# Kernel optimization log

Measured on AMD Instinct MI355X. Metric: run time of the kernel, lower is better.

Reference implementation:

```python
import jax, jax.numpy as jnp
import numpy as np

B, NINP, NCLS = 16384, 2048, 100


def setup_inputs() -> dict:
    key = jax.random.key(0)
    k1, k2, k3, k4, k5 = jax.random.split(key, 5)
    s = 1.0 / np.sqrt(NINP)
    return {
        "time_series": jax.random.normal(k1, (B, NINP), jnp.float32),
        "w_weight": jax.random.uniform(k2, (NINP, NINP), jnp.float32, -s, s),
        "w_bias": jax.random.uniform(k3, (NINP,), jnp.float32, -s, s),
        "fc_weight": jax.random.uniform(k4, (NCLS, NINP), jnp.float32, -s, s),
        "fc_bias": jax.random.uniform(k5, (NCLS,), jnp.float32, -s, s),
    }


def reference(time_series, w_weight, w_bias, fc_weight, fc_bias):
    # time_series: [B, N]
    n = time_series.shape[1]
    # gamma = cumsum(softmax(w(x), axis=1), axis=1): monotone warp in (0, 1]
    gamma = jnp.cumsum(jax.nn.softmax(time_series @ w_weight.T + w_bias, axis=1), axis=1)
    # Interp1d(linspace(0,1,N), x, gamma): per-row linear interpolation,
    # sampling each series at the warped time points gamma.
    xs = jnp.linspace(0.0, 1.0, n, dtype=time_series.dtype)  # shared knot grid
    warped = jax.vmap(lambda g, y: jnp.interp(g, xs, y))(gamma, time_series)  # [B, N]
    return warped @ fc_weight.T + fc_bias  # [B, nclasses]
```

## Files before the change

### kernel.cpp

```cpp
#include <hip/hip_runtime.h>
#include <hip/hip_bf16.h>

#define BROWS 16384
#define NDIM  2048
#define NCLS  100

typedef __attribute__((ext_vector_type(8))) __bf16 bf16x8;
typedef __attribute__((ext_vector_type(4))) float f32x4;
typedef __attribute__((ext_vector_type(4))) unsigned short u16x4;
typedef __attribute__((ext_vector_type(8))) unsigned short u16x8;

__device__ __forceinline__ unsigned short f2bf(float f) {
    union { float f; unsigned int u; } v; v.f = f;
    unsigned int u = v.u;
    unsigned int r = (u + 0x7fffu + ((u >> 16) & 1u)) >> 16;
    return (unsigned short)r;
}
__device__ __forceinline__ float bf2f(unsigned short h) {
    union { unsigned int u; float f; } v; v.u = ((unsigned int)h) << 16;
    return v.f;
}

#define GLOAD_LDS(g, l) \
    __builtin_amdgcn_global_load_lds((const __attribute__((address_space(1))) void*)(g), \
                                     (__attribute__((address_space(3))) void*)(l), 16, 0, 0)

__global__ __launch_bounds__(256) void split_kernel(const float4* __restrict__ src,
                                                    u16x4* __restrict__ hi,
                                                    u16x4* __restrict__ lo, int n4)
{
    int i = blockIdx.x * 256 + threadIdx.x;
    if (i >= n4) return;
    float4 v = src[i];
    u16x4 h, l;
    h.x = f2bf(v.x); l.x = f2bf(v.x - bf2f(h.x));
    h.y = f2bf(v.y); l.y = f2bf(v.y - bf2f(h.y));
    h.z = f2bf(v.z); l.z = f2bf(v.z - bf2f(h.z));
    h.w = f2bf(v.w); l.w = f2bf(v.w - bf2f(h.w));
    hi[i] = h; lo[i] = l;
}

__global__ __launch_bounds__(256) void cvt_bf16_kernel(const float4* __restrict__ src,
                                                       u16x4* __restrict__ dst, int n4)
{
    int i = blockIdx.x * 256 + threadIdx.x;
    if (i >= n4) return;
    float4 v = src[i];
    u16x4 h;
    h.x = f2bf(v.x); h.y = f2bf(v.y); h.z = f2bf(v.z); h.w = f2bf(v.w);
    dst[i] = h;
}

__global__ __launch_bounds__(256) void gemm1_mfma_fused_kernel(
        const unsigned short* __restrict__ xhi,
        const unsigned short* __restrict__ xlo,
        const unsigned short* __restrict__ whi,
        const unsigned short* __restrict__ wlo,
        const float* __restrict__ bias,
        float* __restrict__ C)
{
    __shared__ unsigned short sAh[128 * 32];
    __shared__ unsigned short sAl[128 * 32];
    __shared__ unsigned short sBh[128 * 32];
    __shared__ unsigned short sBl[128 * 32];

    const int tid  = threadIdx.x;
    const int lane = tid & 63;
    const int w    = tid >> 6;
    const int wm   = w & 1;
    const int wn   = w >> 1;
    const int m0   = blockIdx.y * 128;
    const int n0   = blockIdx.x * 128;

    const int c0 = w * 128 + lane;
    const int r0 = c0 >> 2;
    const int q0 = (c0 & 3) ^ ((r0 >> 1) & 3);
    const int c1 = c0 + 64;
    const int r1 = c1 >> 2;
    const int q1 = (c1 & 3) ^ ((r1 >> 1) & 3);

    const size_t a_goff0 = (size_t)(m0 + r0) * NDIM + q0 * 8;
    const size_t a_goff1 = (size_t)(m0 + r1) * NDIM + q1 * 8;
    const size_t b_goff0 = (size_t)(n0 + r0) * NDIM + q0 * 8;
    const size_t b_goff1 = (size_t)(n0 + r1) * NDIM + q1 * 8;

    unsigned short* ldsAh0 = &sAh[w * 1024];   unsigned short* ldsAh1 = &sAh[w * 1024 + 512];
    unsigned short* ldsAl0 = &sAl[w * 1024];   unsigned short* ldsAl1 = &sAl[w * 1024 + 512];
    unsigned short* ldsBh0 = &sBh[w * 1024];   unsigned short* ldsBh1 = &sBh[w * 1024 + 512];
    unsigned short* ldsBl0 = &sBl[w * 1024];   unsigned short* ldsBl1 = &sBl[w * 1024 + 512];

    const int lm = lane & 15;
    const int lk = lane >> 4;
    int offA[4], offB[4];
#pragma unroll
    for (int i = 0; i < 4; i++) {
        int ra = wm * 64 + i * 16 + lm;
        offA[i] = ra * 32 + ((lk ^ ((ra >> 1) & 3)) * 8);
        int rb = wn * 64 + i * 16 + lm;
        offB[i] = rb * 32 + ((lk ^ ((rb >> 1) & 3)) * 8);
    }

    f32x4 acc[4][4];
#pragma unroll
    for (int i = 0; i < 4; i++)
#pragma unroll
        for (int j = 0; j < 4; j++) acc[i][j] = (f32x4){0.f, 0.f, 0.f, 0.f};

    for (int kt = 0; kt < NDIM; kt += 32) {
        GLOAD_LDS(xhi + a_goff0 + kt, ldsAh0);
        GLOAD_LDS(xhi + a_goff1 + kt, ldsAh1);
        GLOAD_LDS(xlo + a_goff0 + kt, ldsAl0);
        GLOAD_LDS(xlo + a_goff1 + kt, ldsAl1);
        GLOAD_LDS(whi + b_goff0 + kt, ldsBh0);
        GLOAD_LDS(whi + b_goff1 + kt, ldsBh1);
        GLOAD_LDS(wlo + b_goff0 + kt, ldsBl0);
        GLOAD_LDS(wlo + b_goff1 + kt, ldsBl1);
        __syncthreads();

        bf16x8 ah[4], al[4], bh[4], bl[4];
#pragma unroll
        for (int i = 0; i < 4; i++) {
            ah[i] = *(const bf16x8*)&sAh[offA[i]];
            al[i] = *(const bf16x8*)&sAl[offA[i]];
            bh[i] = *(const bf16x8*)&sBh[offB[i]];
            bl[i] = *(const bf16x8*)&sBl[offB[i]];
        }
#pragma unroll
        for (int i = 0; i < 4; i++)
#pragma unroll
            for (int j = 0; j < 4; j++) {
                acc[i][j] = __builtin_amdgcn_mfma_f32_16x16x32_bf16(ah[i], bh[j], acc[i][j], 0, 0, 0);
                acc[i][j] = __builtin_amdgcn_mfma_f32_16x16x32_bf16(ah[i], bl[j], acc[i][j], 0, 0, 0);
                acc[i][j] = __builtin_amdgcn_mfma_f32_16x16x32_bf16(al[i], bh[j], acc[i][j], 0, 0, 0);
            }
        __syncthreads();
    }

    const int cn = lane & 15;
    const int rg = lane >> 4;
    float bb[4];
#pragma unroll
    for (int j = 0; j < 4; j++) bb[j] = bias[n0 + wn * 64 + j * 16 + cn];
#pragma unroll
    for (int i = 0; i < 4; i++) {
#pragma unroll
        for (int j = 0; j < 4; j++) {
            const int n = n0 + wn * 64 + j * 16 + cn;
#pragma unroll
            for (int reg = 0; reg < 4; reg++) {
                const int m = m0 + wm * 64 + i * 16 + rg * 4 + reg;
                C[(size_t)m * NDIM + n] = acc[i][j][reg] + bb[j];
            }
        }
    }
}

__global__ __launch_bounds__(256) void warp_bf16_kernel(const float* __restrict__ X,
                                                        const float* __restrict__ L,
                                                        unsigned short* __restrict__ Wout)
{
    const int N = NDIM;
    const int row = blockIdx.x;
    const int tid = threadIdx.x;
    const int lane = tid & 63;
    const int wave = tid >> 6;

    __shared__ float s_x[NDIM];
    __shared__ float s_red[4];
    __shared__ float s_wsum[4];

    const float* lrow = L + (size_t)row * N;
    const float* xrow = X + (size_t)row * N;

    float v[8];
    {
        float4 l0 = *(const float4*)(lrow + tid * 8);
        float4 l1 = *(const float4*)(lrow + tid * 8 + 4);
        v[0] = l0.x; v[1] = l0.y; v[2] = l0.z; v[3] = l0.w;
        v[4] = l1.x; v[5] = l1.y; v[6] = l1.z; v[7] = l1.w;
        float4 x0 = *(const float4*)(xrow + tid * 8);
        float4 x1 = *(const float4*)(xrow + tid * 8 + 4);
        *(float4*)&s_x[tid * 8]     = x0;
        *(float4*)&s_x[tid * 8 + 4] = x1;
    }

    float mx = v[0];
#pragma unroll
    for (int j = 1; j < 8; j++) mx = fmaxf(mx, v[j]);
#pragma unroll
    for (int off = 32; off > 0; off >>= 1) mx = fmaxf(mx, __shfl_down(mx, off));
    if (lane == 0) s_red[wave] = mx;
    __syncthreads();
    mx = fmaxf(fmaxf(s_red[0], s_red[1]), fmaxf(s_red[2], s_red[3]));

    float c = 0.0f;
#pragma unroll
    for (int j = 0; j < 8; j++) {
        float e = __expf(v[j] - mx);
        c += e;
        v[j] = c;
    }

    float sc = c;
#pragma unroll
    for (int off = 1; off < 64; off <<= 1) {
        float t = __shfl_up(sc, off);
        if (lane >= off) sc += t;
    }
    if (lane == 63) s_wsum[wave] = sc;
    __syncthreads();
    float base = 0.0f, total = 0.0f;
#pragma unroll
    for (int w = 0; w < 4; w++) {
        float t = s_wsum[w];
        if (w < wave) base += t;
        total += t;
    }
    const float inv = 1.0f / total;
    const float prefix = base + (sc - c);

    u16x8 o;
#pragma unroll
    for (int j = 0; j < 8; j++) {
        float g = (prefix + v[j]) * inv;
        float pos = g * (float)(N - 1);
        pos = fminf(fmaxf(pos, 0.0f), (float)(N - 1));
        int i = (int)pos;
        if (i > N - 2) i = N - 2;
        float f = pos - (float)i;
        o[j] = f2bf(fmaf(f, s_x[i + 1] - s_x[i], s_x[i]));
    }
    *(u16x8*)(Wout + (size_t)row * N + tid * 8) = o;
}

__global__ __launch_bounds__(256) void gemm2_mfma_kernel(
        const unsigned short* __restrict__ Wp,
        const unsigned short* __restrict__ F,
        const float* __restrict__ fb,
        float* __restrict__ out)
{
    __shared__ unsigned short sA[64 * 32];
    __shared__ unsigned short sB[128 * 32];

    const int tid  = threadIdx.x;
    const int lane = tid & 63;
    const int w    = tid >> 6;
    const int wm   = w & 1;
    const int wn   = w >> 1;
    const int m0   = blockIdx.x * 64;

    const int ca = w * 64 + lane;
    const int ra = ca >> 2;
    const int qa = (ca & 3) ^ ((ra >> 1) & 3);
    const size_t a_goff = (size_t)(m0 + ra) * NDIM + qa * 8;
    unsigned short* ldsA = &sA[w * 512];

    const int cb0 = w * 128 + lane;
    const int rb0 = cb0 >> 2;
    const int qb0 = (cb0 & 3) ^ ((rb0 >> 1) & 3);
    const int cb1 = cb0 + 64;
    const int rb1 = cb1 >> 2;
    const int qb1 = (cb1 & 3) ^ ((rb1 >> 1) & 3);
    const size_t b_goff0 = (size_t)(rb0 < NCLS ? rb0 : NCLS - 1) * NDIM + qb0 * 8;
    const size_t b_goff1 = (size_t)(rb1 < NCLS ? rb1 : NCLS - 1) * NDIM + qb1 * 8;
    unsigned short* ldsB0 = &sB[w * 1024];
    unsigned short* ldsB1 = &sB[w * 1024 + 512];

    const int lm = lane & 15;
    const int lk = lane >> 4;
    int offA[2], offB[4];
#pragma unroll
    for (int i = 0; i < 2; i++) {
        int r = wm * 32 + i * 16 + lm;
        offA[i] = r * 32 + ((lk ^ ((r >> 1) & 3)) * 8);
    }
#pragma unroll
    for (int j = 0; j < 4; j++) {
        int r = wn * 64 + j * 16 + lm;
        offB[j] = r * 32 + ((lk ^ ((r >> 1) & 3)) * 8);
    }

    f32x4 acc[2][4];
#pragma unroll
    for (int i = 0; i < 2; i++)
#pragma unroll
        for (int j = 0; j < 4; j++) acc[i][j] = (f32x4){0.f, 0.f, 0.f, 0.f};

    for (int kt = 0; kt < NDIM; kt += 32) {
        GLOAD_LDS(Wp + a_goff + kt, ldsA);
        GLOAD_LDS(F + b_goff0 + kt, ldsB0);
        GLOAD_LDS(F + b_goff1 + kt, ldsB1);
        __syncthreads();

        bf16x8 af[2], bf[4];
#pragma unroll
        for (int i = 0; i < 2; i++) af[i] = *(const bf16x8*)&sA[offA[i]];
#pragma unroll
        for (int j = 0; j < 4; j++) bf[j] = *(const bf16x8*)&sB[offB[j]];
#pragma unroll
        for (int i = 0; i < 2; i++)
#pragma unroll
            for (int j = 0; j < 4; j++)
                acc[i][j] = __builtin_amdgcn_mfma_f32_16x16x32_bf16(af[i], bf[j], acc[i][j], 0, 0, 0);
        __syncthreads();
    }

    const int cn = lane & 15;
    const int rg = lane >> 4;
#pragma unroll
    for (int i = 0; i < 2; i++) {
#pragma unroll
        for (int j = 0; j < 4; j++) {
            const int n = wn * 64 + j * 16 + cn;
            if (n < NCLS) {
                const float bbn = fb[n];
#pragma unroll
                for (int reg = 0; reg < 4; reg++) {
                    const int m = m0 + wm * 32 + i * 16 + rg * 4 + reg;
                    out[(size_t)m * NCLS + n] = acc[i][j][reg] + bbn;
                }
            }
        }
    }
}

__global__ __launch_bounds__(256) void gemm1_kernel(const float* __restrict__ X,
                                                    const float* __restrict__ W,
                                                    const float* __restrict__ bias,
                                                    float* __restrict__ C)
{
    const int K = NDIM;
    __shared__ float sA[16][128];
    __shared__ float sB[16][128];
    const int tid = threadIdx.x;
    const int tx = tid & 15;
    const int ty = tid >> 4;
    const int m0 = blockIdx.y * 128;
    const int n0 = blockIdx.x * 128;
    float acc[8][8];
#pragma unroll
    for (int i = 0; i < 8; i++)
#pragma unroll
        for (int j = 0; j < 8; j++) acc[i][j] = 0.0f;
    const int s_m = tid >> 1;
    const int s_c = (tid & 1) * 8;
    const float* Ag = X + (size_t)(m0 + s_m) * K + s_c;
    const float* Bg = W + (size_t)(n0 + s_m) * K + s_c;
    for (int kt = 0; kt < K; kt += 16) {
        float4 av0 = *(const float4*)(Ag + kt);
        float4 av1 = *(const float4*)(Ag + kt + 4);
        float4 bv0 = *(const float4*)(Bg + kt);
        float4 bv1 = *(const float4*)(Bg + kt + 4);
        __syncthreads();
        sA[s_c + 0][s_m] = av0.x; sA[s_c + 1][s_m] = av0.y;
        sA[s_c + 2][s_m] = av0.z; sA[s_c + 3][s_m] = av0.w;
        sA[s_c + 4][s_m] = av1.x; sA[s_c + 5][s_m] = av1.y;
        sA[s_c + 6][s_m] = av1.z; sA[s_c + 7][s_m] = av1.w;
        sB[s_c + 0][s_m] = bv0.x; sB[s_c + 1][s_m] = bv0.y;
        sB[s_c + 2][s_m] = bv0.z; sB[s_c + 3][s_m] = bv0.w;
        sB[s_c + 4][s_m] = bv1.x; sB[s_c + 5][s_m] = bv1.y;
        sB[s_c + 6][s_m] = bv1.z; sB[s_c + 7][s_m] = bv1.w;
        __syncthreads();
#pragma unroll
        for (int k = 0; k < 16; k++) {
            float4 a0 = *(const float4*)&sA[k][ty * 8];
            float4 a1 = *(const float4*)&sA[k][ty * 8 + 4];
            float4 b0 = *(const float4*)&sB[k][tx * 8];
            float4 b1 = *(const float4*)&sB[k][tx * 8 + 4];
            float a[8] = {a0.x, a0.y, a0.z, a0.w, a1.x, a1.y, a1.z, a1.w};
            float b[8] = {b0.x, b0.y, b0.z, b0.w, b1.x, b1.y, b1.z, b1.w};
#pragma unroll
            for (int i = 0; i < 8; i++)
#pragma unroll
                for (int j = 0; j < 8; j++)
                    acc[i][j] = fmaf(a[i], b[j], acc[i][j]);
        }
    }
    float bb[8];
#pragma unroll
    for (int j = 0; j < 8; j++) bb[j] = bias[n0 + tx * 8 + j];
#pragma unroll
    for (int i = 0; i < 8; i++) {
        const int m = m0 + ty * 8 + i;
        float* crow = C + (size_t)m * NDIM + n0 + tx * 8;
        *(float4*)(crow)     = make_float4(acc[i][0] + bb[0], acc[i][1] + bb[1],
                                           acc[i][2] + bb[2], acc[i][3] + bb[3]);
        *(float4*)(crow + 4) = make_float4(acc[i][4] + bb[4], acc[i][5] + bb[5],
                                           acc[i][6] + bb[6], acc[i][7] + bb[7]);
    }
}

__global__ __launch_bounds__(256) void warp_kernel_f32(const float* __restrict__ X,
                                                       float* __restrict__ L)
{
    const int N = NDIM;
    const int row = blockIdx.x;
    const int tid = threadIdx.x;
    const int lane = tid & 63;
    const int wave = tid >> 6;
    __shared__ float s_x[NDIM];
    __shared__ float s_red[4];
    __shared__ float s_wsum[4];
    float* lrow = L + (size_t)row * N;
    const float* xrow = X + (size_t)row * N;
    float v[8];
    {
        float4 l0 = *(const float4*)(lrow + tid * 8);
        float4 l1 = *(const float4*)(lrow + tid * 8 + 4);
        v[0] = l0.x; v[1] = l0.y; v[2] = l0.z; v[3] = l0.w;
        v[4] = l1.x; v[5] = l1.y; v[6] = l1.z; v[7] = l1.w;
        float4 x0 = *(const float4*)(xrow + tid * 8);
        float4 x1 = *(const float4*)(xrow + tid * 8 + 4);
        *(float4*)&s_x[tid * 8]     = x0;
        *(float4*)&s_x[tid * 8 + 4] = x1;
    }
    float mx = v[0];
#pragma unroll
    for (int j = 1; j < 8; j++) mx = fmaxf(mx, v[j]);
#pragma unroll
    for (int off = 32; off > 0; off >>= 1) mx = fmaxf(mx, __shfl_down(mx, off));
    if (lane == 0) s_red[wave] = mx;
    __syncthreads();
    mx = fmaxf(fmaxf(s_red[0], s_red[1]), fmaxf(s_red[2], s_red[3]));
    float c = 0.0f;
#pragma unroll
    for (int j = 0; j < 8; j++) {
        float e = __expf(v[j] - mx);
        c += e;
        v[j] = c;
    }
    float sc = c;
#pragma unroll
    for (int off = 1; off < 64; off <<= 1) {
        float t = __shfl_up(sc, off);
        if (lane >= off) sc += t;
    }
    if (lane == 63) s_wsum[wave] = sc;
    __syncthreads();
    float base = 0.0f, total = 0.0f;
#pragma unroll
    for (int w = 0; w < 4; w++) {
        float t = s_wsum[w];
        if (w < wave) base += t;
        total += t;
    }
    const float inv = 1.0f / total;
    const float prefix = base + (sc - c);
    float w8[8];
#pragma unroll
    for (int j = 0; j < 8; j++) {
        float g = (prefix + v[j]) * inv;
        float pos = g * (float)(N - 1);
        pos = fminf(fmaxf(pos, 0.0f), (float)(N - 1));
        int i = (int)pos;
        if (i > N - 2) i = N - 2;
        float f = pos - (float)i;
        w8[j] = fmaf(f, s_x[i + 1] - s_x[i], s_x[i]);
    }
    *(float4*)(lrow + tid * 8)     = make_float4(w8[0], w8[1], w8[2], w8[3]);
    *(float4*)(lrow + tid * 8 + 4) = make_float4(w8[4], w8[5], w8[6], w8[7]);
}

__global__ __launch_bounds__(256) void gemm2_kernel(const float* __restrict__ Wp,
                                                    const float* __restrict__ F,
                                                    const float* __restrict__ fb,
                                                    float* __restrict__ out)
{
    const int K = NDIM;
    __shared__ float sA[16][64];
    __shared__ float sB[16][128];
    const int tid = threadIdx.x;
    const int tx = tid & 15;
    const int ty = tid >> 4;
    const int m0 = blockIdx.x * 64;
    float acc[4][8];
#pragma unroll
    for (int i = 0; i < 4; i++)
#pragma unroll
        for (int j = 0; j < 8; j++) acc[i][j] = 0.0f;
    const int a_m = tid >> 2;
    const int a_c = (tid & 3) * 4;
    const int b_n = tid >> 1;
    const int b_c = (tid & 1) * 8;
    const bool bvalid = (b_n < NCLS);
    const float* Ag = Wp + (size_t)(m0 + a_m) * K + a_c;
    const float* Bg = F + (size_t)b_n * K + b_c;
    for (int kt = 0; kt < K; kt += 16) {
        float4 av = *(const float4*)(Ag + kt);
        float4 bv0 = make_float4(0.f, 0.f, 0.f, 0.f);
        float4 bv1 = make_float4(0.f, 0.f, 0.f, 0.f);
        if (bvalid) {
            bv0 = *(const float4*)(Bg + kt);
            bv1 = *(const float4*)(Bg + kt + 4);
        }
        __syncthreads();
        sA[a_c + 0][a_m] = av.x; sA[a_c + 1][a_m] = av.y;
        sA[a_c + 2][a_m] = av.z; sA[a_c + 3][a_m] = av.w;
        sB[b_c + 0][b_n] = bv0.x; sB[b_c + 1][b_n] = bv0.y;
        sB[b_c + 2][b_n] = bv0.z; sB[b_c + 3][b_n] = bv0.w;
        sB[b_c + 4][b_n] = bv1.x; sB[b_c + 5][b_n] = bv1.y;
        sB[b_c + 6][b_n] = bv1.z; sB[b_c + 7][b_n] = bv1.w;
        __syncthreads();
#pragma unroll
        for (int k = 0; k < 16; k++) {
            float4 a4 = *(const float4*)&sA[k][ty * 4];
            float4 b0 = *(const float4*)&sB[k][tx * 8];
            float4 b1 = *(const float4*)&sB[k][tx * 8 + 4];
            float a[4] = {a4.x, a4.y, a4.z, a4.w};
            float b[8] = {b0.x, b0.y, b0.z, b0.w, b1.x, b1.y, b1.z, b1.w};
#pragma unroll
            for (int i = 0; i < 4; i++)
#pragma unroll
                for (int j = 0; j < 8; j++)
                    acc[i][j] = fmaf(a[i], b[j], acc[i][j]);
        }
    }
#pragma unroll
    for (int i = 0; i < 4; i++) {
        const int m = m0 + ty * 4 + i;
#pragma unroll
        for (int j = 0; j < 8; j++) {
            const int n = tx * 8 + j;
            if (n < NCLS) out[(size_t)m * NCLS + n] = acc[i][j] + fb[n];
        }
    }
}

extern "C" void kernel_launch(void* const* d_in, const int* in_sizes, int n_in,
                              void* d_out, int out_size, void* d_ws, size_t ws_size,
                              hipStream_t stream) {
    const float* x  = (const float*)d_in[0];
    const float* ww = (const float*)d_in[1];
    const float* wb = (const float*)d_in[2];
    const float* fw = (const float*)d_in[3];
    const float* fb = (const float*)d_in[4];
    float* out = (float*)d_out;

    char* ws = (char*)d_ws;
    float* logits = (float*)ws;
    const size_t LOGITS_B = (size_t)BROWS * NDIM * 4;
    const size_t XBF_B    = (size_t)BROWS * NDIM * 2;
    const size_t WBF_B    = (size_t)NDIM * NDIM * 2;
    unsigned short* xhi = (unsigned short*)(ws + LOGITS_B);
    unsigned short* xlo = (unsigned short*)(ws + LOGITS_B + XBF_B);
    unsigned short* whi = (unsigned short*)(ws + LOGITS_B + 2 * XBF_B);
    unsigned short* wlo = (unsigned short*)(ws + LOGITS_B + 2 * XBF_B + WBF_B);
    unsigned short* wbf = xlo;
    unsigned short* fwb = wlo;
    const size_t WS_NEED = LOGITS_B + 2 * XBF_B + 2 * WBF_B;

    if (ws_size >= WS_NEED) {
        split_kernel<<<(BROWS * NDIM / 4 + 255) / 256, 256, 0, stream>>>(
            (const float4*)x, (u16x4*)xhi, (u16x4*)xlo, BROWS * NDIM / 4);
        split_kernel<<<(NDIM * NDIM / 4 + 255) / 256, 256, 0, stream>>>(
            (const float4*)ww, (u16x4*)whi, (u16x4*)wlo, NDIM * NDIM / 4);
        gemm1_mfma_fused_kernel<<<dim3(NDIM / 128, BROWS / 128), 256, 0, stream>>>(
            xhi, xlo, whi, wlo, wb, logits);
        warp_bf16_kernel<<<BROWS, 256, 0, stream>>>(x, logits, wbf);
        cvt_bf16_kernel<<<(NCLS * NDIM / 4 + 255) / 256, 256, 0, stream>>>(
            (const float4*)fw, (u16x4*)fwb, NCLS * NDIM / 4);
        gemm2_mfma_kernel<<<BROWS / 64, 256, 0, stream>>>(wbf, fwb, fb, out);
    } else {
        gemm1_kernel<<<dim3(NDIM / 128, BROWS / 128), 256, 0, stream>>>(x, ww, wb, logits);
        warp_kernel_f32<<<BROWS, 256, 0, stream>>>(x, logits);
        gemm2_kernel<<<BROWS / 64, 256, 0, stream>>>(logits, fw, fb, out);
    }
}
```

Measured before the change: 699.2 us.

## Triple-buffer GEMM1 LDS loads with 32x32 MFMA and merge split kernels

Result: slower. 1.011 ms (+44.6%).

```diff
diff --git a/kernel.cpp b/kernel.cpp
--- a/kernel.cpp
+++ b/kernel.cpp
@@ -7,6 +7,7 @@
 
 typedef __attribute__((ext_vector_type(8))) __bf16 bf16x8;
 typedef __attribute__((ext_vector_type(4))) float f32x4;
+typedef __attribute__((ext_vector_type(16))) float f32x16;
 typedef __attribute__((ext_vector_type(4))) unsigned short u16x4;
 typedef __attribute__((ext_vector_type(8))) unsigned short u16x8;
 
@@ -25,19 +26,25 @@
     __builtin_amdgcn_global_load_lds((const __attribute__((address_space(1))) void*)(g), \
                                      (__attribute__((address_space(3))) void*)(l), 16, 0, 0)
 
-__global__ __launch_bounds__(256) void split_kernel(const float4* __restrict__ src,
-                                                    u16x4* __restrict__ hi,
-                                                    u16x4* __restrict__ lo, int n4)
+#define WAITCNT_VM4 0x0F74
+
+__global__ __launch_bounds__(256) void prep_kernel(const float4* __restrict__ x,
+                                                   const float4* __restrict__ w,
+                                                   u16x4* __restrict__ xhi, u16x4* __restrict__ xlo,
+                                                   u16x4* __restrict__ whi, u16x4* __restrict__ wlo,
+                                                   int n4x, int n4w)
 {
     int i = blockIdx.x * 256 + threadIdx.x;
-    if (i >= n4) return;
-    float4 v = src[i];
+    const float4* src; u16x4 *hi, *lo; int idx;
+    if (i < n4x) { src = x; hi = xhi; lo = xlo; idx = i; }
+    else { idx = i - n4x; if (idx >= n4w) return; src = w; hi = whi; lo = wlo; }
+    float4 v = src[idx];
     u16x4 h, l;
     h.x = f2bf(v.x); l.x = f2bf(v.x - bf2f(h.x));
     h.y = f2bf(v.y); l.y = f2bf(v.y - bf2f(h.y));
     h.z = f2bf(v.z); l.z = f2bf(v.z - bf2f(h.z));
     h.w = f2bf(v.w); l.w = f2bf(v.w - bf2f(h.w));
-    hi[i] = h; lo[i] = l;
+    hi[idx] = h; lo[idx] = l;
 }
 
 __global__ __launch_bounds__(256) void cvt_bf16_kernel(const float4* __restrict__ src,
@@ -51,7 +58,7 @@
     dst[i] = h;
 }
 
-__global__ __launch_bounds__(256) void gemm1_mfma_fused_kernel(
+__global__ __launch_bounds__(256) void gemm1_pipe_kernel(
         const unsigned short* __restrict__ xhi,
         const unsigned short* __restrict__ xlo,
         const unsigned short* __restrict__ whi,
@@ -59,10 +66,10 @@
         const float* __restrict__ bias,
         float* __restrict__ C)
 {
-    __shared__ unsigned short sAh[128 * 32];
-    __shared__ unsigned short sAl[128 * 32];
-    __shared__ unsigned short sBh[128 * 32];
-    __shared__ unsigned short sBl[128 * 32];
+    __shared__ unsigned short sAh[3 * 2048];
+    __shared__ unsigned short sAl[3 * 2048];
+    __shared__ unsigned short sBh[3 * 2048];
+    __shared__ unsigned short sBl[3 * 2048];
 
     const int tid  = threadIdx.x;
     const int lane = tid & 63;
@@ -72,83 +79,87 @@
     const int m0   = blockIdx.y * 128;
     const int n0   = blockIdx.x * 128;
 
-    const int c0 = w * 128 + lane;
-    const int r0 = c0 >> 2;
-    const int q0 = (c0 & 3) ^ ((r0 >> 1) & 3);
-    const int c1 = c0 + 64;
-    const int r1 = c1 >> 2;
-    const int q1 = (c1 & 3) ^ ((r1 >> 1) & 3);
-
-    const size_t a_goff0 = (size_t)(m0 + r0) * NDIM + q0 * 8;
-    const size_t a_goff1 = (size_t)(m0 + r1) * NDIM + q1 * 8;
-    const size_t b_goff0 = (size_t)(n0 + r0) * NDIM + q0 * 8;
-    const size_t b_goff1 = (size_t)(n0 + r1) * NDIM + q1 * 8;
-
-    unsigned short* ldsAh0 = &sAh[w * 1024];   unsigned short* ldsAh1 = &sAh[w * 1024 + 512];
-    unsigned short* ldsAl0 = &sAl[w * 1024];   unsigned short* ldsAl1 = &sAl[w * 1024 + 512];
-    unsigned short* ldsBh0 = &sBh[w * 1024];   unsigned short* ldsBh1 = &sBh[w * 1024 + 512];
-    unsigned short* ldsBl0 = &sBl[w * 1024];   unsigned short* ldsBl1 = &sBl[w * 1024 + 512];
-
-    const int lm = lane & 15;
-    const int lk = lane >> 4;
-    int offA[4], offB[4];
-#pragma unroll
-    for (int i = 0; i < 4; i++) {
-        int ra = wm * 64 + i * 16 + lm;
-        offA[i] = ra * 32 + ((lk ^ ((ra >> 1) & 3)) * 8);
-        int rb = wn * 64 + i * 16 + lm;
-        offB[i] = rb * 32 + ((lk ^ ((rb >> 1) & 3)) * 8);
-    }
-
-    f32x4 acc[4][4];
-#pragma unroll
-    for (int i = 0; i < 4; i++)
-#pragma unroll
-        for (int j = 0; j < 4; j++) acc[i][j] = (f32x4){0.f, 0.f, 0.f, 0.f};
-
-    for (int kt = 0; kt < NDIM; kt += 32) {
-        GLOAD_LDS(xhi + a_goff0 + kt, ldsAh0);
-        GLOAD_LDS(xhi + a_goff1 + kt, ldsAh1);
-        GLOAD_LDS(xlo + a_goff0 + kt, ldsAl0);
-        GLOAD_LDS(xlo + a_goff1 + kt, ldsAl1);
-        GLOAD_LDS(whi + b_goff0 + kt, ldsBh0);
-        GLOAD_LDS(whi + b_goff1 + kt, ldsBh1);
-        GLOAD_LDS(wlo + b_goff0 + kt, ldsBl0);
-        GLOAD_LDS(wlo + b_goff1 + kt, ldsBl1);
-        __syncthreads();
-
-        bf16x8 ah[4], al[4], bh[4], bl[4];
-#pragma unroll
-        for (int i = 0; i < 4; i++) {
-            ah[i] = *(const bf16x8*)&sAh[offA[i]];
-            al[i] = *(const bf16x8*)&sAl[offA[i]];
-            bh[i] = *(const bf16x8*)&sBh[offB[i]];
-            bl[i] = *(const bf16x8*)&sBl[offB[i]];
-        }
-#pragma unroll
-        for (int i = 0; i < 4; i++)
-#pragma unroll
-            for (int j = 0; j < 4; j++) {
-                acc[i][j] = __builtin_amdgcn_mfma_f32_16x16x32_bf16(ah[i], bh[j], acc[i][j], 0, 0, 0);
-                acc[i][j] = __builtin_amdgcn_mfma_f32_16x16x32_bf16(ah[i], bl[j], acc[i][j], 0, 0, 0);
-                acc[i][j] = __builtin_amdgcn_mfma_f32_16x16x32_bf16(al[i], bh[j], acc[i][j], 0, 0, 0);
+    const int cc = w * 64 + lane;
+    const int sq = cc >> 7;
+    const int sr = cc & 127;
+    const size_t a_goff = (size_t)(m0 + sr) * NDIM + sq * 8;
+    const size_t b_goff = (size_t)(n0 + sr) * NDIM + sq * 8;
+    const int lds_off = w * 512;
+
+    const int ln32 = lane & 31;
+    const int lk2  = lane >> 5;
+    const int offA0 = (lk2 * 128 + wm * 64 +  0 + ln32) * 8;
+    const int offA1 = (lk2 * 128 + wm * 64 + 32 + ln32) * 8;
+    const int offB0 = (lk2 * 128 + wn * 64 +  0 + ln32) * 8;
+    const int offB1 = (lk2 * 128 + wn * 64 + 32 + ln32) * 8;
+
+    f32x16 acc[2][2];
+#pragma unroll
+    for (int i = 0; i < 2; i++)
+#pragma unroll
+        for (int j = 0; j < 2; j++)
+#pragma unroll
+            for (int r = 0; r < 16; r++) acc[i][j][r] = 0.f;
+
+    GLOAD_LDS(xhi + a_goff +  0, &sAh[lds_off]);
+    GLOAD_LDS(xlo + a_goff +  0, &sAl[lds_off]);
+    GLOAD_LDS(whi + b_goff +  0, &sBh[lds_off]);
+    GLOAD_LDS(wlo + b_goff +  0, &sBl[lds_off]);
+    GLOAD_LDS(xhi + a_goff + 16, &sAh[2048 + lds_off]);
+    GLOAD_LDS(xlo + a_goff + 16, &sAl[2048 + lds_off]);
+    GLOAD_LDS(whi + b_goff + 16, &sBh[2048 + lds_off]);
+    GLOAD_LDS(wlo + b_goff + 16, &sBl[2048 + lds_off]);
+
+    int st = 0;
+    int sn = 2;
+    for (int k = 0; k < 128; ++k) {
+        __builtin_amdgcn_s_waitcnt(WAITCNT_VM4);
+        __builtin_amdgcn_s_barrier();
+
+        {
+            const int kn = ((k + 2) & 127) * 16;
+            const int so = sn * 2048 + lds_off;
+            GLOAD_LDS(xhi + a_goff + kn, &sAh[so]);
+            GLOAD_LDS(xlo + a_goff + kn, &sAl[so]);
+            GLOAD_LDS(whi + b_goff + kn, &sBh[so]);
+            GLOAD_LDS(wlo + b_goff + kn, &sBl[so]);
+        }
+
+        const int sb = st * 2048;
+        bf16x8 ah[2], al[2], bh[2], bl[2];
+        ah[0] = *(const bf16x8*)&sAh[sb + offA0];
+        ah[1] = *(const bf16x8*)&sAh[sb + offA1];
+        al[0] = *(const bf16x8*)&sAl[sb + offA0];
+        al[1] = *(const bf16x8*)&sAl[sb + offA1];
+        bh[0] = *(const bf16x8*)&sBh[sb + offB0];
+        bh[1] = *(const bf16x8*)&sBh[sb + offB1];
+        bl[0] = *(const bf16x8*)&sBl[sb + offB0];
+        bl[1] = *(const bf16x8*)&sBl[sb + offB1];
+
+#pragma unroll
+        for (int i = 0; i < 2; i++)
+#pragma unroll
+            for (int j = 0; j < 2; j++) {
+                acc[i][j] = __builtin_amdgcn_mfma_f32_32x32x16_bf16(ah[i], bh[j], acc[i][j], 0, 0, 0);
+                acc[i][j] = __builtin_amdgcn_mfma_f32_32x32x16_bf16(ah[i], bl[j], acc[i][j], 0, 0, 0);
+                acc[i][j] = __builtin_amdgcn_mfma_f32_32x32x16_bf16(al[i], bh[j], acc[i][j], 0, 0, 0);
             }
-        __syncthreads();
-    }
-
-    const int cn = lane & 15;
-    const int rg = lane >> 4;
-    float bb[4];
-#pragma unroll
-    for (int j = 0; j < 4; j++) bb[j] = bias[n0 + wn * 64 + j * 16 + cn];
-#pragma unroll
-    for (int i = 0; i < 4; i++) {
-#pragma unroll
-        for (int j = 0; j < 4; j++) {
-            const int n = n0 + wn * 64 + j * 16 + cn;
-#pragma unroll
-            for (int reg = 0; reg < 4; reg++) {
-                const int m = m0 + wm * 64 + i * 16 + rg * 4 + reg;
+
+        st = (st == 2) ? 0 : st + 1;
+        sn = (sn == 2) ? 0 : sn + 1;
+    }
+
+    float bb[2];
+#pragma unroll
+    for (int j = 0; j < 2; j++) bb[j] = bias[n0 + wn * 64 + j * 32 + ln32];
+#pragma unroll
+    for (int i = 0; i < 2; i++) {
+#pragma unroll
+        for (int j = 0; j < 2; j++) {
+            const int n = n0 + wn * 64 + j * 32 + ln32;
+#pragma unroll
+            for (int reg = 0; reg < 16; reg++) {
+                const int m = m0 + wm * 64 + i * 32 + (reg & 3) + 8 * (reg >> 2) + 4 * lk2;
                 C[(size_t)m * NDIM + n] = acc[i][j][reg] + bb[j];
             }
         }
@@ -550,11 +561,12 @@
     const size_t WS_NEED = LOGITS_B + 2 * XBF_B + 2 * WBF_B;
 
     if (ws_size >= WS_NEED) {
-        split_kernel<<<(BROWS * NDIM / 4 + 255) / 256, 256, 0, stream>>>(
-            (const float4*)x, (u16x4*)xhi, (u16x4*)xlo, BROWS * NDIM / 4);
-        split_kernel<<<(NDIM * NDIM / 4 + 255) / 256, 256, 0, stream>>>(
-            (const float4*)ww, (u16x4*)whi, (u16x4*)wlo, NDIM * NDIM / 4);
-        gemm1_mfma_fused_kernel<<<dim3(NDIM / 128, BROWS / 128), 256, 0, stream>>>(
+        const int n4x = BROWS * NDIM / 4;
+        const int n4w = NDIM * NDIM / 4;
+        prep_kernel<<<(n4x + n4w + 255) / 256, 256, 0, stream>>>(
+            (const float4*)x, (const float4*)ww,
+            (u16x4*)xhi, (u16x4*)xlo, (u16x4*)whi, (u16x4*)wlo, n4x, n4w);
+        gemm1_pipe_kernel<<<dim3(NDIM / 128, BROWS / 128), 256, 0, stream>>>(
             xhi, xlo, whi, wlo, wb, logits);
         warp_bf16_kernel<<<BROWS, 256, 0, stream>>>(x, logits, wbf);
         cvt_bf16_kernel<<<(NCLS * NDIM / 4 + 255) / 256, 256, 0, stream>>>(
```
